# Kernel optimization log

Hardware: AMD Instinct MI355X
Metric: run time of the kernel (lower is better)

Reference implementation:

```python
import jax, jax.numpy as jnp
import numpy as np

D = 256          # d_model
NPRE = 16; NMLP = 16; NPOST = 16
K = 4            # top_k
P = NPRE * NMLP * NPOST   # 4096 pathways
HMAX = 5 * D     # max mlp expert hidden width (padded storage)
B, S = 8, 256


def _gelu(z):
    return jax.nn.gelu(z, approximate=False)  # torch nn.GELU default = exact erf


def _ln(z, g, b, eps=1e-5):
    mu = z.mean(-1, keepdims=True)
    v = ((z - mu) ** 2).mean(-1, keepdims=True)
    return (z - mu) * jax.lax.rsqrt(v + eps) * g + b


def setup_inputs() -> dict:
    key = jax.random.key(0)
    ks = jax.random.split(key, 8)

    def nrm(k, shape, scale):
        return jax.random.normal(k, shape, dtype=jnp.float32) * scale

    return {
        "x": nrm(ks[0], (B, S, D), 1.0),
        # router MLP (dropout inactive in eval)
        "rw1": nrm(ks[1], (D, 256), D ** -0.5), "rb1": jnp.zeros((256,), jnp.float32),
        "rw2": nrm(ks[2], (256, 128), 256 ** -0.5), "rb2": jnp.zeros((128,), jnp.float32),
        "rw3": nrm(ks[3], (128, P), 128 ** -0.5), "rb3": jnp.zeros((P,), jnp.float32),
        "temp": jnp.ones((1,), jnp.float32),
        # pre experts: Linear + LayerNorm + act
        "pw": nrm(ks[4], (NPRE, D, D), D ** -0.5), "pb": jnp.zeros((NPRE, D), jnp.float32),
        "pg": jnp.ones((NPRE, D), jnp.float32), "pbb": jnp.zeros((NPRE, D), jnp.float32),
        # mlp experts: variable hidden D*(2+i//4), padded to HMAX (unused cols sliced off)
        "mw1": nrm(ks[5], (NMLP, D, HMAX), D ** -0.5), "mb1": jnp.zeros((NMLP, HMAX), jnp.float32),
        "mw2": nrm(ks[6], (NMLP, HMAX, D), HMAX ** -0.5), "mb2": jnp.zeros((NMLP, D), jnp.float32),
        # post experts: Linear + (LayerNorm if even)
        "qw": nrm(ks[7], (NPOST, D, D), D ** -0.5), "qb": jnp.zeros((NPOST, D), jnp.float32),
        "qg": jnp.ones((NPOST, D), jnp.float32), "qbb": jnp.zeros((NPOST, D), jnp.float32),
    }


def reference(x, rw1, rb1, rw2, rb2, rw3, rb3, temp, pw, pb, pg, pbb,
              mw1, mb1, mw2, mb2, qw, qb, qg, qbb):
    Bv, Sv, Dv = x.shape
    N = Bv * Sv
    xt = x.reshape(N, Dv)

    # ---- router ----
    h = _gelu(xt @ rw1 + rb1)
    h = _gelu(h @ rw2 + rb2)
    scores = h @ rw3 + rb3                                  # [N, P]

    # ---- GLBL load-balance loss (softmax without temperature; torch.var unbiased) ----
    freq = jax.nn.softmax(scores, axis=-1).mean(0)          # [P]
    glbl_loss = P * jnp.var(freq, ddof=1)

    # ---- top-k pathway selection ----
    probs = jax.nn.softmax(scores / temp[0], axis=-1)
    top_vals, top_idx = jax.lax.top_k(probs, K)             # [N, K]
    pw_full = jnp.zeros((N, P), x.dtype).at[jnp.arange(N)[:, None], top_idx].set(top_vals)
    pathway_weights = pw_full / (pw_full.sum(-1, keepdims=True) + 1e-8)

    # ---- decompose pathway index -> (pre, mlp, post) ----
    pre_idx = top_idx // (NMLP * NPOST)
    rem = top_idx % (NMLP * NPOST)
    mlp_idx = rem // NPOST
    post_idx = rem % NPOST

    # ---- pre experts: compute all, gather per (token, slot) ----
    acts = [_gelu, jax.nn.relu, jnp.tanh]
    pre_all = jnp.stack(
        [acts[i % 3](_ln(xt @ pw[i] + pb[i], pg[i], pbb[i])) for i in range(NPRE)],
        axis=1)                                              # [N, NPRE, D]
    x_pre = jnp.take_along_axis(pre_all, pre_idx[:, :, None], axis=1)  # [N, K, D]

    # ---- mlp experts (variable hidden width), masked combine ----
    x_mlp = jnp.zeros_like(x_pre)
    for j in range(NMLP):
        hid = Dv * (2 + j // 4)
        a = _gelu if j % 2 == 0 else jax.nn.relu
        mid = a(jnp.einsum('nkd,dh->nkh', x_pre, mw1[j, :, :hid]) + mb1[j, :hid])
        out = jnp.einsum('nkh,hd->nkd', mid, mw2[j, :hid, :]) + mb2[j]
        x_mlp = x_mlp + jnp.where((mlp_idx == j)[:, :, None], out, 0.0)

    # ---- post experts, masked combine ----
    x_post = jnp.zeros_like(x_mlp)
    for q in range(NPOST):
        out = jnp.einsum('nkd,de->nke', x_mlp, qw[q]) + qb[q]
        if q % 2 == 0:
            out = _ln(out, qg[q], qbb[q])
        x_post = x_post + jnp.where((post_idx == q)[:, :, None], out, 0.0)

    # original weights each pathway by its (unnormalized) top value
    output = (x_post * top_vals[:, :, None]).sum(1).reshape(Bv, Sv, Dv)
    return output, glbl_loss, pathway_weights.reshape(Bv, Sv, P)
```

## Files before the change

### kernel.cpp

```cpp
#include <hip/hip_runtime.h>
#include <math.h>

#define DMODEL 256
#define PWAYS  4096
#define TOPK   4
#define HMAX   1280
#define NTOK   2048
#define NPAIR  (NTOK*TOPK)
#define FSLOTS 16
#define MROWS  64
#define YMLP   8
#define CTOT   56

typedef __attribute__((ext_vector_type(8))) short bf16x8;
typedef __attribute__((ext_vector_type(8))) unsigned short u16x8;
typedef __attribute__((ext_vector_type(4))) float f32x4;

#define MFMA_BF16 __builtin_amdgcn_mfma_f32_16x16x32_bf16

__device__ __forceinline__ float gelu_exact(float z) {
    return 0.5f * z * (1.0f + erff(z * 0.70710678118654752440f));
}

__device__ __forceinline__ unsigned short f32_to_bf16_rne(float f) {
    unsigned u = __float_as_uint(f);
    unsigned r = u + 0x7FFFu + ((u >> 16) & 1u);
    return (unsigned short)(r >> 16);
}

__device__ __forceinline__ float bf16_to_f32(unsigned short h) {
    return __uint_as_float((unsigned)h << 16);
}

__device__ __forceinline__ int chunk_base(int e) {
    int g = e >> 2, r = e & 3;
    return 4 * (2 * g + (g * (g - 1)) / 2) + r * (2 + g);
}


__global__ void k_zero(float* __restrict__ pwout, float* __restrict__ freq_part) {
    const int i = blockIdx.x * 256 + threadIdx.x;
    const int stride = gridDim.x * 256;
    for (int j = i; j < NTOK * PWAYS; j += stride) pwout[j] = 0.0f;
    for (int j = i; j < FSLOTS * PWAYS; j += stride) freq_part[j] = 0.0f;
}

__global__ void k_zero2(float* __restrict__ out, float* __restrict__ x_mlp,
                        int* __restrict__ cnts) {
    const int i = blockIdx.x * 256 + threadIdx.x;
    const int stride = gridDim.x * 256;
    for (int j = i; j < NTOK * DMODEL; j += stride) out[j] = 0.0f;
    for (int j = i; j < NPAIR * DMODEL; j += stride) x_mlp[j] = 0.0f;
    if (i < 192) cnts[i] = 0;
}

__global__ void __launch_bounds__(256) k_router_h(
    const float* __restrict__ x,
    const float* __restrict__ rw1, const float* __restrict__ rb1,
    const float* __restrict__ rw2, const float* __restrict__ rb2,
    unsigned short* __restrict__ h2h, unsigned short* __restrict__ h2l,
    unsigned short* __restrict__ xth, unsigned short* __restrict__ xtl) {
    __shared__ float xs[4][DMODEL];
    __shared__ float h1s[4][DMODEL];
    __shared__ float h2s[4][128];
    const int tid = threadIdx.x;
    const int n0 = blockIdx.x * 4;

    for (int idx = tid; idx < 4 * DMODEL; idx += 256) {
        const float v = x[(size_t)n0 * DMODEL + idx];
        xs[idx >> 8][idx & 255] = v;
        const unsigned short h = f32_to_bf16_rne(v);
        xth[(size_t)n0 * DMODEL + idx] = h;
        xtl[(size_t)n0 * DMODEL + idx] = f32_to_bf16_rne(v - bf16_to_f32(h));
    }
    __syncthreads();

    {
        float bias = rb1[tid];
        float a0 = bias, a1 = bias, a2 = bias, a3 = bias;
        for (int c = 0; c < DMODEL; c++) {
            float wv = rw1[c * DMODEL + tid];
            a0 += xs[0][c] * wv; a1 += xs[1][c] * wv;
            a2 += xs[2][c] * wv; a3 += xs[3][c] * wv;
        }
        h1s[0][tid] = gelu_exact(a0); h1s[1][tid] = gelu_exact(a1);
        h1s[2][tid] = gelu_exact(a2); h1s[3][tid] = gelu_exact(a3);
    }
    __syncthreads();

    {
        const int col = tid & 127;
        const int pr = tid >> 7;
        float bias = rb2[col];
        float b0 = bias, b1 = bias;
        for (int c = 0; c < DMODEL; c++) {
            float wv = rw2[c * 128 + col];
            b0 += h1s[2 * pr + 0][c] * wv;
            b1 += h1s[2 * pr + 1][c] * wv;
        }
        h2s[2 * pr + 0][col] = gelu_exact(b0);
        h2s[2 * pr + 1][col] = gelu_exact(b1);
    }
    __syncthreads();

    for (int idx = tid; idx < 512; idx += 256) {
        const int t = idx >> 7, col = idx & 127;
        const float v = h2s[t][col];
        const unsigned short h = f32_to_bf16_rne(v);
        const size_t o = (size_t)(n0 + t) * 128 + col;
        h2h[o] = h;
        h2l[o] = f32_to_bf16_rne(v - bf16_to_f32(h));
    }
}

__global__ void __launch_bounds__(256) k_pack3(
    const float* __restrict__ rw3, unsigned short* __restrict__ P3) {
    const int nb = blockIdx.x;
    const int tid = threadIdx.x;
    const int kb = tid >> 6, lane = tid & 63;
    const int l15 = lane & 15, lhi = lane >> 4;
    const int k0 = kb * 32 + lhi * 8;
    const int n = nb * 16 + l15;
    u16x8 hv, lv;
#pragma unroll
    for (int j = 0; j < 8; ++j) {
        const float f = rw3[(size_t)(k0 + j) * PWAYS + n];
        const unsigned short h = f32_to_bf16_rne(f);
        hv[j] = h;
        lv[j] = f32_to_bf16_rne(f - bf16_to_f32(h));
    }
    const size_t o0 = ((size_t)(0 * 256 + nb) * 4 + kb) * 512 + (size_t)lane * 8;
    const size_t o1 = ((size_t)(1 * 256 + nb) * 4 + kb) * 512 + (size_t)lane * 8;
    *(u16x8*)&P3[o0] = hv;
    *(u16x8*)&P3[o1] = lv;
}

__global__ void __launch_bounds__(256) k_packq(
    const float* __restrict__ pw, const float* __restrict__ qw,
    unsigned short* __restrict__ PPK, unsigned short* __restrict__ QPK) {
    const int e = blockIdx.x;
    const int which = blockIdx.y;
    const int kb = blockIdx.z;
    const int tid = threadIdx.x;
    const int wid = tid >> 6, lane = tid & 63;
    const int l15 = lane & 15, lhi = lane >> 4;
    const float* src = which ? qw : pw;
    unsigned short* dst = which ? QPK : PPK;

    for (int nb = wid; nb < 16; nb += 4) {
        const int n = nb * 16 + l15;
        const int k0 = kb * 32 + lhi * 8;
        u16x8 hv, lv;
#pragma unroll
        for (int j = 0; j < 8; ++j) {
            const float f = src[(size_t)e * DMODEL * DMODEL + (size_t)(k0 + j) * DMODEL + n];
            const unsigned short h = f32_to_bf16_rne(f);
            hv[j] = h;
            lv[j] = f32_to_bf16_rne(f - bf16_to_f32(h));
        }
        const size_t o0 = ((((size_t)e * 2 + 0) * 16 + nb) * 8 + kb) * 512 + (size_t)lane * 8;
        const size_t o1 = ((((size_t)e * 2 + 1) * 16 + nb) * 8 + kb) * 512 + (size_t)lane * 8;
        *(u16x8*)&dst[o0] = hv;
        *(u16x8*)&dst[o1] = lv;
    }
}

__global__ void __launch_bounds__(256, 2) k_scores(
    const unsigned short* __restrict__ h2h, const unsigned short* __restrict__ h2l,
    const unsigned short* __restrict__ P3, const float* __restrict__ rb3,
    float* __restrict__ scores) {
    const int n0 = blockIdx.x * 32;
    const int by = blockIdx.y;
    const int tid = threadIdx.x;
    const int wid = tid >> 6, lane = tid & 63;
    const int l15 = lane & 15, lhi = lane >> 4;

    __shared__ unsigned short ah[32][136];
    __shared__ unsigned short al[32][136];

    for (int t = tid; t < 512; t += 256) {
        const int row = t >> 4, seg = (t & 15) * 8;
        const size_t g = (size_t)(n0 + row) * 128 + seg;
        *(u16x8*)&ah[row][seg] = *(const u16x8*)&h2h[g];
        *(u16x8*)&al[row][seg] = *(const u16x8*)&h2l[g];
    }
    __syncthreads();

    f32x4 acc[2][4];
    const f32x4 zf = {0.f, 0.f, 0.f, 0.f};
#pragma unroll
    for (int ms = 0; ms < 2; ++ms)
#pragma unroll
        for (int ns = 0; ns < 4; ++ns) acc[ms][ns] = zf;

#pragma unroll 1
    for (int kb = 0; kb < 4; ++kb) {
        const int ko = kb * 32 + lhi * 8;
        const bf16x8 a_h0 = *(const bf16x8*)&ah[l15][ko];
        const bf16x8 a_h1 = *(const bf16x8*)&ah[16 + l15][ko];
        const bf16x8 a_l0 = *(const bf16x8*)&al[l15][ko];
        const bf16x8 a_l1 = *(const bf16x8*)&al[16 + l15][ko];
#pragma unroll
        for (int ns = 0; ns < 4; ++ns) {
            const int nb = by * 16 + wid * 4 + ns;
            const size_t bo = ((size_t)nb * 4 + kb) * 512 + (size_t)lane * 8;
            const bf16x8 bh = *(const bf16x8*)&P3[bo];
            const bf16x8 bl = *(const bf16x8*)&P3[bo + 524288];
            acc[0][ns] = MFMA_BF16(a_h0, bh, acc[0][ns], 0, 0, 0);
            acc[1][ns] = MFMA_BF16(a_h1, bh, acc[1][ns], 0, 0, 0);
            acc[0][ns] = MFMA_BF16(a_l0, bh, acc[0][ns], 0, 0, 0);
            acc[1][ns] = MFMA_BF16(a_l1, bh, acc[1][ns], 0, 0, 0);
            acc[0][ns] = MFMA_BF16(a_h0, bl, acc[0][ns], 0, 0, 0);
            acc[1][ns] = MFMA_BF16(a_h1, bl, acc[1][ns], 0, 0, 0);
        }
    }

#pragma unroll
    for (int ms = 0; ms < 2; ++ms)
#pragma unroll
        for (int ns = 0; ns < 4; ++ns) {
            const int col = by * 256 + wid * 64 + ns * 16 + l15;
            const float bias = rb3[col];
#pragma unroll
            for (int r = 0; r < 4; ++r) {
                const int row = n0 + ms * 16 + lhi * 4 + r;
                scores[(size_t)row * PWAYS + col] = acc[ms][ns][r] + bias;
            }
        }
}

__global__ void __launch_bounds__(256) k_topk(
    const float* __restrict__ scores, const float* __restrict__ temp,
    int* __restrict__ top_idx, float* __restrict__ top_vals,
    float* __restrict__ pw_out, float* __restrict__ tok_m, float* __restrict__ tok_i) {
    const int n = blockIdx.x;
    const int tid = threadIdx.x;
    const int wid = tid >> 6, lane = tid & 63;
    const float* row = scores + (size_t)n * PWAYS;

    float sv[16];
#pragma unroll
    for (int i = 0; i < 16; ++i) sv[i] = row[tid + i * 256];

    __shared__ float wred[4];
    __shared__ float wr1[4], wrT[4];
    __shared__ float wbv[4];
    __shared__ int wbi[4];
    __shared__ int sel[TOPK];
    __shared__ float selv[TOPK];

    float lmax = -3.402823466e38f;
#pragma unroll
    for (int i = 0; i < 16; ++i) lmax = fmaxf(lmax, sv[i]);
    for (int o = 32; o > 0; o >>= 1) lmax = fmaxf(lmax, __shfl_down(lmax, o));
    if (lane == 0) wred[wid] = lmax;
    __syncthreads();
    const float m = fmaxf(fmaxf(wred[0], wred[1]), fmaxf(wred[2], wred[3]));

    const float invT = 1.0f / temp[0];
    float e1 = 0.f, eT = 0.f;
#pragma unroll
    for (int i = 0; i < 16; ++i) {
        const float d = sv[i] - m;
        e1 += expf(d);
        eT += expf(d * invT);
    }
    for (int o = 32; o > 0; o >>= 1) { e1 += __shfl_down(e1, o); eT += __shfl_down(eT, o); }
    if (lane == 0) { wr1[wid] = e1; wrT[wid] = eT; }
    __syncthreads();
    const float sum1 = wr1[0] + wr1[1] + wr1[2] + wr1[3];
    const float sumT = wrT[0] + wrT[1] + wrT[2] + wrT[3];

    for (int r = 0; r < TOPK; ++r) {
        float bv = -3.402823466e38f;
        int bi = PWAYS;
#pragma unroll
        for (int i = 0; i < 16; ++i) {
            const int p = tid + i * 256;
            bool skip = false;
            for (int u = 0; u < r; ++u) if (sel[u] == p) skip = true;
            if (!skip && sv[i] > bv) { bv = sv[i]; bi = p; }
        }
        for (int o = 32; o > 0; o >>= 1) {
            const float ov = __shfl_down(bv, o);
            const int oi = __shfl_down(bi, o);
            if (ov > bv || (ov == bv && oi < bi)) { bv = ov; bi = oi; }
        }
        if (lane == 0) { wbv[wid] = bv; wbi[wid] = bi; }
        __syncthreads();
        if (tid == 0) {
            float b = wbv[0]; int bidx = wbi[0];
            for (int w = 1; w < 4; ++w)
                if (wbv[w] > b || (wbv[w] == b && wbi[w] < bidx)) { b = wbv[w]; bidx = wbi[w]; }
            sel[r] = bidx; selv[r] = b;
        }
        __syncthreads();
    }

    if (tid == 0) {
        float tv[TOPK];
        float wsum = 1e-8f;
#pragma unroll
        for (int k2 = 0; k2 < TOPK; ++k2) {
            tv[k2] = expf((selv[k2] - m) * invT) / sumT;
            wsum += tv[k2];
        }
        const float invw = 1.0f / wsum;
#pragma unroll
        for (int k2 = 0; k2 < TOPK; ++k2) {
            top_idx[n * TOPK + k2] = sel[k2];
            top_vals[n * TOPK + k2] = tv[k2];
            pw_out[(size_t)n * PWAYS + sel[k2]] = tv[k2] * invw;
        }
        tok_m[n] = m;
        tok_i[n] = 1.0f / sum1;
    }
}

__global__ void __launch_bounds__(256) k_freq(
    const float* __restrict__ scores, const float* __restrict__ tok_m,
    const float* __restrict__ tok_i, float* __restrict__ freq_part) {
    const int bx = blockIdx.x;
    const int by = blockIdx.y;
    const int tid = threadIdx.x;
    const int wid = tid >> 6, lane = tid & 63;
    const int col = bx * 64 + lane;

    float acc = 0.f;
    const int r0 = by * 128;
    for (int r = r0 + wid; r < r0 + 128; r += 4) {
        const float mm = tok_m[r], iv = tok_i[r];
        acc += expf(scores[(size_t)r * PWAYS + col] - mm) * iv;
    }
    __shared__ float fs[4][64];
    fs[wid][lane] = acc;
    __syncthreads();
    if (wid == 0)
        freq_part[(size_t)by * PWAYS + col] = fs[0][lane] + fs[1][lane] + fs[2][lane] + fs[3][lane];
}

__global__ void k_freq_loss(const float* __restrict__ freq_part, float* __restrict__ out_loss) {
    __shared__ float fl[PWAYS];
    __shared__ float red[256];
    const int tid = threadIdx.x;
    for (int p = tid; p < PWAYS; p += 256) {
        float s = 0.f;
        for (int sl = 0; sl < FSLOTS; sl++) s += freq_part[(size_t)sl * PWAYS + p];
        fl[p] = s * (1.0f / NTOK);
    }
    __syncthreads();
    float s = 0.f;
    for (int p = tid; p < PWAYS; p += 256) s += fl[p];
    red[tid] = s; __syncthreads();
    for (int st = 128; st > 0; st >>= 1) { if (tid < st) red[tid] += red[tid + st]; __syncthreads(); }
    const float mu = red[0] * (1.0f / PWAYS);
    __syncthreads();
    float ss = 0.f;
    for (int p = tid; p < PWAYS; p += 256) {
        float d = fl[p] - mu;
        ss += d * d;
    }
    red[tid] = ss; __syncthreads();
    for (int st = 128; st > 0; st >>= 1) { if (tid < st) red[tid] += red[tid + st]; __syncthreads(); }
    if (tid == 0)
        out_loss[0] = (float)PWAYS * red[0] / (float)(PWAYS - 1);
}


__global__ void k_count(const int* __restrict__ top_idx, int* __restrict__ counts) {
    const int p = blockIdx.x * 256 + threadIdx.x;
    if (p >= NPAIR) return;
    const int idx = top_idx[p];
    atomicAdd(&counts[0 * 16 + (idx >> 8)], 1);
    atomicAdd(&counts[1 * 16 + ((idx >> 4) & 15)], 1);
    atomicAdd(&counts[2 * 16 + (idx & 15)], 1);
}

__global__ void k_prefix(const int* __restrict__ counts, int* __restrict__ offsets,
                         int* __restrict__ cursors) {
    if (threadIdx.x != 0 || blockIdx.x != 0) return;
    for (int s = 0; s < 3; s++) {
        int run = 0;
        for (int e = 0; e < 16; e++) {
            offsets[s * 16 + e] = run;
            cursors[s * 16 + e] = run;
            run += counts[s * 16 + e];
        }
    }
}

__global__ void k_scatter(const int* __restrict__ top_idx, int* __restrict__ cursors,
                          int* __restrict__ lists) {
    const int p = blockIdx.x * 256 + threadIdx.x;
    if (p >= NPAIR) return;
    const int idx = top_idx[p];
    int pos;
    pos = atomicAdd(&cursors[0 * 16 + (idx >> 8)], 1);        lists[0 * NPAIR + pos] = p;
    pos = atomicAdd(&cursors[1 * 16 + ((idx >> 4) & 15)], 1); lists[1 * NPAIR + pos] = p;
    pos = atomicAdd(&cursors[2 * 16 + (idx & 15)], 1);        lists[2 * NPAIR + pos] = p;
}

__global__ void __launch_bounds__(256) k_packw(
    const float* __restrict__ mw1, const float* __restrict__ mw2,
    unsigned short* __restrict__ W1P, unsigned short* __restrict__ W2P) {
    const int cl = blockIdx.x;
    const int which = blockIdx.y;
    const int kb = blockIdx.z;
    int e = 0;
    while (e < 15 && chunk_base(e + 1) <= cl) ++e;
    const int ch = cl - chunk_base(e);
    const int hbase = ch * 256;
    const int tid = threadIdx.x;
    const int wid = tid >> 6, lane = tid & 63;
    const int l15 = lane & 15, lhi = lane >> 4;

    unsigned short* dst = which ? W2P : W1P;

    for (int nb = wid; nb < 16; nb += 4) {
        const int n = nb * 16 + l15;
        const int k0 = kb * 32 + lhi * 8;
        u16x8 hv, lv;
#pragma unroll
        for (int j = 0; j < 8; ++j) {
            float f;
            if (which == 0)
                f = mw1[((size_t)e * DMODEL + (k0 + j)) * HMAX + hbase + n];
            else
                f = mw2[((size_t)e * HMAX + hbase + k0 + j) * DMODEL + n];
            const unsigned short h = f32_to_bf16_rne(f);
            hv[j] = h;
            lv[j] = f32_to_bf16_rne(f - bf16_to_f32(h));
        }
        const size_t o0 = ((((size_t)cl * 2 + 0) * 16 + nb) * 8 + kb) * 512 + (size_t)lane * 8;
        const size_t o1 = ((((size_t)cl * 2 + 1) * 16 + nb) * 8 + kb) * 512 + (size_t)lane * 8;
        *(u16x8*)&dst[o0] = hv;
        *(u16x8*)&dst[o1] = lv;
    }
}

__global__ void __launch_bounds__(256) k_cvt(
    const float* __restrict__ src, unsigned short* __restrict__ dh,
    unsigned short* __restrict__ dl) {
    const size_t i = ((size_t)blockIdx.x * 256 + threadIdx.x) * 4;
    const float4 v = *(const float4*)&src[i];
    ushort4 hv, lv;
    hv.x = f32_to_bf16_rne(v.x); lv.x = f32_to_bf16_rne(v.x - bf16_to_f32(hv.x));
    hv.y = f32_to_bf16_rne(v.y); lv.y = f32_to_bf16_rne(v.y - bf16_to_f32(hv.y));
    hv.z = f32_to_bf16_rne(v.z); lv.z = f32_to_bf16_rne(v.z - bf16_to_f32(hv.z));
    hv.w = f32_to_bf16_rne(v.w); lv.w = f32_to_bf16_rne(v.w - bf16_to_f32(hv.w));
    *(ushort4*)&dh[i] = hv;
    *(ushort4*)&dl[i] = lv;
}

__global__ void __launch_bounds__(256, 2) k_pre_mfma(
    const unsigned short* __restrict__ xth, const unsigned short* __restrict__ xtl,
    const unsigned short* __restrict__ PPK,
    const float* __restrict__ pb, const float* __restrict__ pg, const float* __restrict__ pbb,
    const int* __restrict__ counts, const int* __restrict__ offsets,
    const int* __restrict__ lists,
    unsigned short* __restrict__ x_h, unsigned short* __restrict__ x_l) {
    const int e = blockIdx.x;
    const int cnt = counts[e];
    if (cnt == 0) return;
    const int off = offsets[e];
    const int am = e % 3;
    const int tid = threadIdx.x;
    const int wid = tid >> 6, lane = tid & 63;
    const int l15 = lane & 15, lhi = lane >> 4;

    __shared__ int prs[32];
    __shared__ unsigned short ah[32][264];
    __shared__ unsigned short al[32][264];
    __shared__ float s1s[4][32], s2s[4][32];
    __shared__ float mus[32], ivs[32];

    float bias4[4], g4[4], bb4[4];
#pragma unroll
    for (int ns = 0; ns < 4; ++ns) {
        const int col = wid * 64 + ns * 16 + l15;
        bias4[ns] = pb[e * DMODEL + col];
        g4[ns] = pg[e * DMODEL + col];
        bb4[ns] = pbb[e * DMODEL + col];
    }
    const size_t wbase = (size_t)e * 2 * 65536;

    for (int base = blockIdx.y * 32; base < cnt; base += 16 * 32) {
        const int Tact = min(32, cnt - base);
        if (tid < 32) prs[tid] = lists[off + base + min(tid, Tact - 1)];
        __syncthreads();
        for (int t = tid; t < 1024; t += 256) {
            const int row = t >> 5, seg = (t & 31) * 8;
            const size_t gsrc = (size_t)(prs[row] >> 2) * DMODEL + seg;
            *(uint4*)&ah[row][seg] = *(const uint4*)&xth[gsrc];
            *(uint4*)&al[row][seg] = *(const uint4*)&xtl[gsrc];
        }
        __syncthreads();

        f32x4 acc[2][4];
        const f32x4 zf = {0.f, 0.f, 0.f, 0.f};
#pragma unroll
        for (int ms = 0; ms < 2; ++ms)
#pragma unroll
            for (int ns = 0; ns < 4; ++ns) acc[ms][ns] = zf;

#pragma unroll 1
        for (int kb = 0; kb < 8; ++kb) {
            const int ko = kb * 32 + lhi * 8;
            const bf16x8 a_h0 = *(const bf16x8*)&ah[l15][ko];
            const bf16x8 a_h1 = *(const bf16x8*)&ah[16 + l15][ko];
            const bf16x8 a_l0 = *(const bf16x8*)&al[l15][ko];
            const bf16x8 a_l1 = *(const bf16x8*)&al[16 + l15][ko];
#pragma unroll
            for (int ns = 0; ns < 4; ++ns) {
                const size_t bo = wbase + (size_t)(((wid * 4 + ns) * 8 + kb) * 512 + lane * 8);
                const bf16x8 bh = *(const bf16x8*)&PPK[bo];
                const bf16x8 bl = *(const bf16x8*)&PPK[bo + 65536];
                acc[0][ns] = MFMA_BF16(a_h0, bh, acc[0][ns], 0, 0, 0);
                acc[1][ns] = MFMA_BF16(a_h1, bh, acc[1][ns], 0, 0, 0);
                acc[0][ns] = MFMA_BF16(a_l0, bh, acc[0][ns], 0, 0, 0);
                acc[1][ns] = MFMA_BF16(a_l1, bh, acc[1][ns], 0, 0, 0);
                acc[0][ns] = MFMA_BF16(a_h0, bl, acc[0][ns], 0, 0, 0);
                acc[1][ns] = MFMA_BF16(a_h1, bl, acc[1][ns], 0, 0, 0);
            }
        }

#pragma unroll
        for (int ms = 0; ms < 2; ++ms)
#pragma unroll
            for (int r = 0; r < 4; ++r) {
                float s1 = 0.f, s2 = 0.f;
#pragma unroll
                for (int ns = 0; ns < 4; ++ns) {
                    const float v = acc[ms][ns][r] + bias4[ns];
                    s1 += v; s2 += v * v;
                }
#pragma unroll
                for (int o = 1; o < 16; o <<= 1) {
                    s1 += __shfl_xor(s1, o);
                    s2 += __shfl_xor(s2, o);
                }
                if (l15 == 0) {
                    s1s[wid][ms * 16 + lhi * 4 + r] = s1;
                    s2s[wid][ms * 16 + lhi * 4 + r] = s2;
                }
            }
        __syncthreads();
        if (tid < 32) {
            const float s1 = s1s[0][tid] + s1s[1][tid] + s1s[2][tid] + s1s[3][tid];
            const float s2 = s2s[0][tid] + s2s[1][tid] + s2s[2][tid] + s2s[3][tid];
            const float mu = s1 * (1.0f / DMODEL);
            mus[tid] = mu;
            ivs[tid] = rsqrtf(s2 * (1.0f / DMODEL) - mu * mu + 1e-5f);
        }
        __syncthreads();

#pragma unroll
        for (int ms = 0; ms < 2; ++ms)
#pragma unroll
            for (int ns = 0; ns < 4; ++ns) {
                const int col = wid * 64 + ns * 16 + l15;
#pragma unroll
                for (int r = 0; r < 4; ++r) {
                    const int row = ms * 16 + lhi * 4 + r;
                    if (row < Tact) {
                        const float v = acc[ms][ns][r] + bias4[ns];
                        float y = (v - mus[row]) * ivs[row] * g4[ns] + bb4[ns];
                        y = (am == 0) ? gelu_exact(y) : (am == 1 ? fmaxf(y, 0.f) : tanhf(y));
                        const unsigned short h = f32_to_bf16_rne(y);
                        const size_t o = (size_t)prs[row] * DMODEL + col;
                        x_h[o] = h;
                        x_l[o] = f32_to_bf16_rne(y - bf16_to_f32(h));
                    }
                }
            }
        __syncthreads();
    }
}

__global__ void __launch_bounds__(256, 2) k_mlp_mfma(
    const unsigned short* __restrict__ x_h, const unsigned short* __restrict__ x_l,
    const unsigned short* __restrict__ W1P, const unsigned short* __restrict__ W2P,
    const float* __restrict__ mb1, const float* __restrict__ mb2,
    const int* __restrict__ counts, const int* __restrict__ offsets,
    const int* __restrict__ lists, float* __restrict__ x_mlp) {
    const int p = blockIdx.x & 7;
    const int j = blockIdx.x >> 3;
    const int ea = p;
    const int eb = (p < 4) ? (p + 12) : (p + 4);
    const int na = (2 + (ea >> 2)) * YMLP;
    int e, ch, y;
    if (j < na) { e = ea; ch = j >> 3; y = j & 7; }
    else        { e = eb; ch = (j - na) >> 3; y = (j - na) & 7; }

    const int cnt = counts[16 + e];
    if (cnt == 0) return;
    const int off = offsets[16 + e];
    const int cl = chunk_base(e) + ch;
    const bool is_gelu = ((e & 1) == 0);
    const int tid = threadIdx.x;
    const int wid = tid >> 6, lane = tid & 63;
    const int l15 = lane & 15, lhi = lane >> 4;

    __shared__ int prs[MROWS];
    __shared__ unsigned short ah[MROWS][264];
    __shared__ unsigned short al[MROWS][264];

    float hb_s[4], ob_s[4];
#pragma unroll
    for (int ns = 0; ns < 4; ++ns) {
        const int col = wid * 64 + ns * 16 + l15;
        hb_s[ns] = mb1[e * HMAX + ch * DMODEL + col];
        ob_s[ns] = (ch == 0) ? mb2[e * DMODEL + col] : 0.0f;
    }

    const size_t wbase = (size_t)cl * 2 * 65536;

    for (int base = y * MROWS; base < cnt; base += YMLP * MROWS) {
        const int Tact = min(MROWS, cnt - base);
        if (tid < MROWS) prs[tid] = lists[NPAIR + off + base + min(tid, Tact - 1)];
        __syncthreads();
        for (int t = tid; t < 2048; t += 256) {
            const int row = t >> 5, seg = (t & 31) * 8;
            const size_t gsrc = (size_t)prs[row] * DMODEL + seg;
            *(uint4*)&ah[row][seg] = *(const uint4*)&x_h[gsrc];
            *(uint4*)&al[row][seg] = *(const uint4*)&x_l[gsrc];
        }
        __syncthreads();

        {
            f32x4 acc[4][4];
            const f32x4 zf = {0.f, 0.f, 0.f, 0.f};
#pragma unroll
            for (int ms = 0; ms < 4; ++ms)
#pragma unroll
                for (int ns = 0; ns < 4; ++ns) acc[ms][ns] = zf;

#pragma unroll 1
            for (int kb = 0; kb < 8; ++kb) {
                const int ko = kb * 32 + lhi * 8;
#pragma unroll
                for (int ns = 0; ns < 4; ++ns) {
                    const size_t bo = wbase + (size_t)(((wid * 4 + ns) * 8 + kb) * 512 + lane * 8);
                    const bf16x8 bh = *(const bf16x8*)&W1P[bo];
                    const bf16x8 bl = *(const bf16x8*)&W1P[bo + 65536];
#pragma unroll
                    for (int ms = 0; ms < 4; ++ms) {
                        const bf16x8 a_h = *(const bf16x8*)&ah[ms * 16 + l15][ko];
                        const bf16x8 a_l = *(const bf16x8*)&al[ms * 16 + l15][ko];
                        acc[ms][ns] = MFMA_BF16(a_h, bh, acc[ms][ns], 0, 0, 0);
                        acc[ms][ns] = MFMA_BF16(a_l, bh, acc[ms][ns], 0, 0, 0);
                        acc[ms][ns] = MFMA_BF16(a_h, bl, acc[ms][ns], 0, 0, 0);
                    }
                }
            }
            __syncthreads();

#pragma unroll
            for (int ms = 0; ms < 4; ++ms)
#pragma unroll
                for (int ns = 0; ns < 4; ++ns) {
                    const int col = wid * 64 + ns * 16 + l15;
#pragma unroll
                    for (int r = 0; r < 4; ++r) {
                        const int row = ms * 16 + lhi * 4 + r;
                        float v = acc[ms][ns][r] + hb_s[ns];
                        v = is_gelu ? gelu_exact(v) : fmaxf(v, 0.0f);
                        const unsigned short h = f32_to_bf16_rne(v);
                        ah[row][col] = h;
                        al[row][col] = f32_to_bf16_rne(v - bf16_to_f32(h));
                    }
                }
            __syncthreads();
        }

        {
            f32x4 acc2[4][4];
            const f32x4 zf = {0.f, 0.f, 0.f, 0.f};
#pragma unroll
            for (int ms = 0; ms < 4; ++ms)
#pragma unroll
                for (int ns = 0; ns < 4; ++ns) acc2[ms][ns] = zf;

#pragma unroll 1
            for (int kb = 0; kb < 8; ++kb) {
                const int ko = kb * 32 + lhi * 8;
#pragma unroll
                for (int ns = 0; ns < 4; ++ns) {
                    const size_t bo = wbase + (size_t)(((wid * 4 + ns) * 8 + kb) * 512 + lane * 8);
                    const bf16x8 bh = *(const bf16x8*)&W2P[bo];
                    const bf16x8 bl = *(const bf16x8*)&W2P[bo + 65536];
#pragma unroll
                    for (int ms = 0; ms < 4; ++ms) {
                        const bf16x8 a_h = *(const bf16x8*)&ah[ms * 16 + l15][ko];
                        const bf16x8 a_l = *(const bf16x8*)&al[ms * 16 + l15][ko];
                        acc2[ms][ns] = MFMA_BF16(a_h, bh, acc2[ms][ns], 0, 0, 0);
                        acc2[ms][ns] = MFMA_BF16(a_l, bh, acc2[ms][ns], 0, 0, 0);
                        acc2[ms][ns] = MFMA_BF16(a_h, bl, acc2[ms][ns], 0, 0, 0);
                    }
                }
            }

#pragma unroll
            for (int ms = 0; ms < 4; ++ms)
#pragma unroll
                for (int ns = 0; ns < 4; ++ns) {
                    const int col = wid * 64 + ns * 16 + l15;
#pragma unroll
                    for (int r = 0; r < 4; ++r) {
                        const int row = ms * 16 + lhi * 4 + r;
                        if (row < Tact)
                            atomicAdd(&x_mlp[(size_t)prs[row] * DMODEL + col],
                                      acc2[ms][ns][r] + ob_s[ns]);
                    }
                }
        }
        __syncthreads();
    }
}

__global__ void __launch_bounds__(256, 2) k_post_mfma(
    const unsigned short* __restrict__ xmh, const unsigned short* __restrict__ xml,
    const unsigned short* __restrict__ QPK,
    const float* __restrict__ qb, const float* __restrict__ qg, const float* __restrict__ qbb,
    const float* __restrict__ top_val,
    const int* __restrict__ counts, const int* __restrict__ offsets,
    const int* __restrict__ lists, float* __restrict__ out) {
    const int e = blockIdx.x;
    const int cnt = counts[32 + e];
    if (cnt == 0) return;
    const int off = offsets[32 + e];
    const bool has_ln = ((e & 1) == 0);
    const int tid = threadIdx.x;
    const int wid = tid >> 6, lane = tid & 63;
    const int l15 = lane & 15, lhi = lane >> 4;

    __shared__ int prs[32];
    __shared__ float tvs[32];
    __shared__ unsigned short ah[32][264];
    __shared__ unsigned short al[32][264];
    __shared__ float s1s[4][32], s2s[4][32];
    __shared__ float mus[32], ivs[32];

    float bias4[4], g4[4], bb4[4];
#pragma unroll
    for (int ns = 0; ns < 4; ++ns) {
        const int col = wid * 64 + ns * 16 + l15;
        bias4[ns] = qb[e * DMODEL + col];
        g4[ns] = qg[e * DMODEL + col];
        bb4[ns] = qbb[e * DMODEL + col];
    }
    const size_t wbase = (size_t)e * 2 * 65536;

    for (int base = blockIdx.y * 32; base < cnt; base += 16 * 32) {
        const int Tact = min(32, cnt - base);
        if (tid < 32) {
            const int p = lists[2 * NPAIR + off + base + min(tid, Tact - 1)];
            prs[tid] = p;
            tvs[tid] = top_val[p];
        }
        __syncthreads();
        for (int t = tid; t < 1024; t += 256) {
            const int row = t >> 5, seg = (t & 31) * 8;
            const size_t gsrc = (size_t)prs[row] * DMODEL + seg;
            *(uint4*)&ah[row][seg] = *(const uint4*)&xmh[gsrc];
            *(uint4*)&al[row][seg] = *(const uint4*)&xml[gsrc];
        }
        __syncthreads();

        f32x4 acc[2][4];
        const f32x4 zf = {0.f, 0.f, 0.f, 0.f};
#pragma unroll
        for (int ms = 0; ms < 2; ++ms)
#pragma unroll
            for (int ns = 0; ns < 4; ++ns) acc[ms][ns] = zf;

#pragma unroll 1
        for (int kb = 0; kb < 8; ++kb) {
            const int ko = kb * 32 + lhi * 8;
            const bf16x8 a_h0 = *(const bf16x8*)&ah[l15][ko];
            const bf16x8 a_h1 = *(const bf16x8*)&ah[16 + l15][ko];
            const bf16x8 a_l0 = *(const bf16x8*)&al[l15][ko];
            const bf16x8 a_l1 = *(const bf16x8*)&al[16 + l15][ko];
#pragma unroll
            for (int ns = 0; ns < 4; ++ns) {
                const size_t bo = wbase + (size_t)(((wid * 4 + ns) * 8 + kb) * 512 + lane * 8);
                const bf16x8 bh = *(const bf16x8*)&QPK[bo];
                const bf16x8 bl = *(const bf16x8*)&QPK[bo + 65536];
                acc[0][ns] = MFMA_BF16(a_h0, bh, acc[0][ns], 0, 0, 0);
                acc[1][ns] = MFMA_BF16(a_h1, bh, acc[1][ns], 0, 0, 0);
                acc[0][ns] = MFMA_BF16(a_l0, bh, acc[0][ns], 0, 0, 0);
                acc[1][ns] = MFMA_BF16(a_l1, bh, acc[1][ns], 0, 0, 0);
                acc[0][ns] = MFMA_BF16(a_h0, bl, acc[0][ns], 0, 0, 0);
                acc[1][ns] = MFMA_BF16(a_h1, bl, acc[1][ns], 0, 0, 0);
            }
        }

        if (has_ln) {
#pragma unroll
            for (int ms = 0; ms < 2; ++ms)
#pragma unroll
                for (int r = 0; r < 4; ++r) {
                    float s1 = 0.f, s2 = 0.f;
#pragma unroll
                    for (int ns = 0; ns < 4; ++ns) {
                        const float v = acc[ms][ns][r] + bias4[ns];
                        s1 += v; s2 += v * v;
                    }
#pragma unroll
                    for (int o = 1; o < 16; o <<= 1) {
                        s1 += __shfl_xor(s1, o);
                        s2 += __shfl_xor(s2, o);
                    }
                    if (l15 == 0) {
                        s1s[wid][ms * 16 + lhi * 4 + r] = s1;
                        s2s[wid][ms * 16 + lhi * 4 + r] = s2;
                    }
                }
            __syncthreads();
            if (tid < 32) {
                const float s1 = s1s[0][tid] + s1s[1][tid] + s1s[2][tid] + s1s[3][tid];
                const float s2 = s2s[0][tid] + s2s[1][tid] + s2s[2][tid] + s2s[3][tid];
                const float mu = s1 * (1.0f / DMODEL);
                mus[tid] = mu;
                ivs[tid] = rsqrtf(s2 * (1.0f / DMODEL) - mu * mu + 1e-5f);
            }
            __syncthreads();
        }

#pragma unroll
        for (int ms = 0; ms < 2; ++ms)
#pragma unroll
            for (int ns = 0; ns < 4; ++ns) {
                const int col = wid * 64 + ns * 16 + l15;
#pragma unroll
                for (int r = 0; r < 4; ++r) {
                    const int row = ms * 16 + lhi * 4 + r;
                    if (row < Tact) {
                        const float v = acc[ms][ns][r] + bias4[ns];
                        const float t = has_ln ? ((v - mus[row]) * ivs[row] * g4[ns] + bb4[ns]) : v;
                        atomicAdd(&out[(size_t)(prs[row] >> 2) * DMODEL + col], tvs[row] * t);
                    }
                }
            }
        __syncthreads();
    }
}

extern "C" void kernel_launch(void* const* d_in, const int* in_sizes, int n_in,
                              void* d_out, int out_size, void* d_ws, size_t ws_size,
                              hipStream_t stream) {
    (void)in_sizes; (void)n_in; (void)out_size; (void)ws_size;

    const float* x    = (const float*)d_in[0];
    const float* rw1  = (const float*)d_in[1];
    const float* rb1  = (const float*)d_in[2];
    const float* rw2  = (const float*)d_in[3];
    const float* rb2  = (const float*)d_in[4];
    const float* rw3  = (const float*)d_in[5];
    const float* rb3  = (const float*)d_in[6];
    const float* temp = (const float*)d_in[7];
    const float* pw   = (const float*)d_in[8];
    const float* pb   = (const float*)d_in[9];
    const float* pg   = (const float*)d_in[10];
    const float* pbb  = (const float*)d_in[11];
    const float* mw1  = (const float*)d_in[12];
    const float* mb1  = (const float*)d_in[13];
    const float* mw2  = (const float*)d_in[14];
    const float* mb2  = (const float*)d_in[15];
    const float* qw   = (const float*)d_in[16];
    const float* qb   = (const float*)d_in[17];
    const float* qg   = (const float*)d_in[18];
    const float* qbb  = (const float*)d_in[19];

    float* out      = (float*)d_out;
    float* out_loss = out + (size_t)NTOK * DMODEL;
    float* out_pw   = out_loss + 1;

    float* freq_part = (float*)d_ws;
    int*   top_idx   = (int*)(freq_part + (size_t)FSLOTS * PWAYS);
    float* top_val   = (float*)(top_idx + NPAIR);
    int*   counts    = (int*)(top_val + NPAIR);
    int*   offsets   = counts + 64;
    int*   cursors   = offsets + 64;
    int*   lists     = cursors + 64;
    float* x_mlp     = (float*)(lists + 3 * NPAIR);
    unsigned short* x_h = (unsigned short*)(x_mlp + (size_t)NPAIR * DMODEL);
    unsigned short* x_l = x_h + (size_t)NPAIR * DMODEL;
    unsigned short* W1P = x_l + (size_t)NPAIR * DMODEL;
    unsigned short* W2P = W1P + (size_t)CTOT * 2 * 65536;
    unsigned short* P3  = W2P + (size_t)CTOT * 2 * 65536;
    unsigned short* h2h = P3 + 2 * 524288;
    unsigned short* h2l = h2h + (size_t)NTOK * 128;
    float* tok_m = (float*)(h2l + (size_t)NTOK * 128);
    float* tok_i = tok_m + NTOK;
    unsigned short* xth = (unsigned short*)(tok_i + NTOK);
    unsigned short* xtl = xth + (size_t)NTOK * DMODEL;
    unsigned short* xmh = xtl + (size_t)NTOK * DMODEL;
    unsigned short* xml = xmh + (size_t)NPAIR * DMODEL;
    unsigned short* PPK = xml + (size_t)NPAIR * DMODEL;
    unsigned short* QPK = PPK + (size_t)16 * 2 * 65536;
    float* scores = x_mlp;

    k_zero<<<1024, 256, 0, stream>>>(out_pw, freq_part);
    k_router_h<<<NTOK / 4, 256, 0, stream>>>(x, rw1, rb1, rw2, rb2, h2h, h2l, xth, xtl);
    k_pack3<<<256, 256, 0, stream>>>(rw3, P3);
    k_packq<<<dim3(16, 2, 8), 256, 0, stream>>>(pw, qw, PPK, QPK);
    k_scores<<<dim3(64, 16), 256, 0, stream>>>(h2h, h2l, P3, rb3, scores);
    k_topk<<<NTOK, 256, 0, stream>>>(scores, temp, top_idx, top_val, out_pw, tok_m, tok_i);
    k_freq<<<dim3(64, 16), 256, 0, stream>>>(scores, tok_m, tok_i, freq_part);
    k_freq_loss<<<1, 256, 0, stream>>>(freq_part, out_loss);

    k_zero2<<<1024, 256, 0, stream>>>(out, x_mlp, counts);
    k_count<<<NPAIR / 256, 256, 0, stream>>>(top_idx, counts);
    k_prefix<<<1, 64, 0, stream>>>(counts, offsets, cursors);
    k_scatter<<<NPAIR / 256, 256, 0, stream>>>(top_idx, cursors, lists);
    k_packw<<<dim3(CTOT, 2, 8), 256, 0, stream>>>(mw1, mw2, W1P, W2P);
    k_pre_mfma<<<dim3(16, 16), 256, 0, stream>>>(xth, xtl, PPK, pb, pg, pbb,
                                                 counts, offsets, lists, x_h, x_l);
    k_mlp_mfma<<<CTOT * YMLP, 256, 0, stream>>>(x_h, x_l, W1P, W2P, mb1, mb2,
                                                counts, offsets, lists, x_mlp);
    k_cvt<<<NPAIR * DMODEL / 1024, 256, 0, stream>>>(x_mlp, xmh, xml);
    k_post_mfma<<<dim3(16, 16), 256, 0, stream>>>(xmh, xml, QPK, qb, qg, qbb, top_val,
                                                  counts, offsets, lists, out);
}
```

Measured before the change: 518.8 us.

## Move router MLP to split-bf16 MFMA and fuse zeroing and conversion passes

The scalar fp32 router hidden layers are replaced with a split-bf16 (hi/lo) MFMA kernel, backed by new packing kernels for rw1/rw2 and a separate x conversion kernel. The zero-fill kernel for the pathway-weight output is dropped; the top-k kernel now writes each full output row, zeros included. The standalone x_mlp bf16 conversion pass is folded into the post-expert kernel's operand staging. The aim is to remove memory passes and slow scalar FMAs, at the cost of extra packing launches and the small error of the split-bf16 approximation.

```diff
diff --git a/kernel.cpp b/kernel.cpp
--- a/kernel.cpp
+++ b/kernel.cpp
@@ -38,13 +38,6 @@
 }
 
 
-__global__ void k_zero(float* __restrict__ pwout, float* __restrict__ freq_part) {
-    const int i = blockIdx.x * 256 + threadIdx.x;
-    const int stride = gridDim.x * 256;
-    for (int j = i; j < NTOK * PWAYS; j += stride) pwout[j] = 0.0f;
-    for (int j = i; j < FSLOTS * PWAYS; j += stride) freq_part[j] = 0.0f;
-}
-
 __global__ void k_zero2(float* __restrict__ out, float* __restrict__ x_mlp,
                         int* __restrict__ cnts) {
     const int i = blockIdx.x * 256 + threadIdx.x;
@@ -54,62 +47,168 @@
     if (i < 192) cnts[i] = 0;
 }
 
-__global__ void __launch_bounds__(256) k_router_h(
-    const float* __restrict__ x,
-    const float* __restrict__ rw1, const float* __restrict__ rb1,
-    const float* __restrict__ rw2, const float* __restrict__ rb2,
-    unsigned short* __restrict__ h2h, unsigned short* __restrict__ h2l,
-    unsigned short* __restrict__ xth, unsigned short* __restrict__ xtl) {
-    __shared__ float xs[4][DMODEL];
-    __shared__ float h1s[4][DMODEL];
-    __shared__ float h2s[4][128];
-    const int tid = threadIdx.x;
-    const int n0 = blockIdx.x * 4;
-
-    for (int idx = tid; idx < 4 * DMODEL; idx += 256) {
-        const float v = x[(size_t)n0 * DMODEL + idx];
-        xs[idx >> 8][idx & 255] = v;
-        const unsigned short h = f32_to_bf16_rne(v);
-        xth[(size_t)n0 * DMODEL + idx] = h;
-        xtl[(size_t)n0 * DMODEL + idx] = f32_to_bf16_rne(v - bf16_to_f32(h));
+__global__ void __launch_bounds__(256) k_cvtx(
+    const float* __restrict__ src, unsigned short* __restrict__ dh,
+    unsigned short* __restrict__ dl) {
+    const size_t i = ((size_t)blockIdx.x * 256 + threadIdx.x) * 4;
+    const float4 v = *(const float4*)&src[i];
+    ushort4 hv, lv;
+    hv.x = f32_to_bf16_rne(v.x); lv.x = f32_to_bf16_rne(v.x - bf16_to_f32(hv.x));
+    hv.y = f32_to_bf16_rne(v.y); lv.y = f32_to_bf16_rne(v.y - bf16_to_f32(hv.y));
+    hv.z = f32_to_bf16_rne(v.z); lv.z = f32_to_bf16_rne(v.z - bf16_to_f32(hv.z));
+    hv.w = f32_to_bf16_rne(v.w); lv.w = f32_to_bf16_rne(v.w - bf16_to_f32(hv.w));
+    *(ushort4*)&dh[i] = hv;
+    *(ushort4*)&dl[i] = lv;
+}
+
+__global__ void __launch_bounds__(256) k_pack12(
+    const float* __restrict__ rw1, const float* __restrict__ rw2,
+    unsigned short* __restrict__ R1P, unsigned short* __restrict__ R2P) {
+    const int bx = blockIdx.x;
+    const int tid = threadIdx.x;
+    const int kq = tid >> 6, lane = tid & 63;
+    const int l15 = lane & 15, lhi = lane >> 4;
+    const bool is1 = (bx < 16);
+    const int nb = is1 ? bx : (bx - 16);
+    const int N = is1 ? 256 : 128;
+    const float* src = is1 ? rw1 : rw2;
+    unsigned short* dst = is1 ? R1P : R2P;
+    const int nblk = is1 ? 16 : 8;
+    const int pstride = nblk * 8 * 512;
+    const int n = nb * 16 + l15;
+
+    for (int k2 = 0; k2 < 2; ++k2) {
+        const int kb = kq + k2 * 4;
+        const int k0 = kb * 32 + lhi * 8;
+        u16x8 hv, lv;
+#pragma unroll
+        for (int j = 0; j < 8; ++j) {
+            const float f = src[(size_t)(k0 + j) * N + n];
+            const unsigned short h = f32_to_bf16_rne(f);
+            hv[j] = h;
+            lv[j] = f32_to_bf16_rne(f - bf16_to_f32(h));
+        }
+        const size_t o = ((size_t)nb * 8 + kb) * 512 + (size_t)lane * 8;
+        *(u16x8*)&dst[o] = hv;
+        *(u16x8*)&dst[o + pstride] = lv;
+    }
+}
+
+__global__ void __launch_bounds__(256, 2) k_h12(
+    const unsigned short* __restrict__ xth, const unsigned short* __restrict__ xtl,
+    const unsigned short* __restrict__ R1P, const unsigned short* __restrict__ R2P,
+    const float* __restrict__ rb1, const float* __restrict__ rb2,
+    unsigned short* __restrict__ h2h, unsigned short* __restrict__ h2l) {
+    const int n0 = blockIdx.x * 32;
+    const int tid = threadIdx.x;
+    const int wid = tid >> 6, lane = tid & 63;
+    const int l15 = lane & 15, lhi = lane >> 4;
+
+    __shared__ unsigned short ah[32][264];
+    __shared__ unsigned short al[32][264];
+
+    for (int t = tid; t < 1024; t += 256) {
+        const int row = t >> 5, seg = (t & 31) * 8;
+        const size_t g = (size_t)(n0 + row) * DMODEL + seg;
+        *(u16x8*)&ah[row][seg] = *(const u16x8*)&xth[g];
+        *(u16x8*)&al[row][seg] = *(const u16x8*)&xtl[g];
     }
     __syncthreads();
 
     {
-        float bias = rb1[tid];
-        float a0 = bias, a1 = bias, a2 = bias, a3 = bias;
-        for (int c = 0; c < DMODEL; c++) {
-            float wv = rw1[c * DMODEL + tid];
-            a0 += xs[0][c] * wv; a1 += xs[1][c] * wv;
-            a2 += xs[2][c] * wv; a3 += xs[3][c] * wv;
-        }
-        h1s[0][tid] = gelu_exact(a0); h1s[1][tid] = gelu_exact(a1);
-        h1s[2][tid] = gelu_exact(a2); h1s[3][tid] = gelu_exact(a3);
-    }
-    __syncthreads();
+        f32x4 acc[2][4];
+        const f32x4 zf = {0.f, 0.f, 0.f, 0.f};
+#pragma unroll
+        for (int ms = 0; ms < 2; ++ms)
+#pragma unroll
+            for (int ns = 0; ns < 4; ++ns) acc[ms][ns] = zf;
+
+#pragma unroll 1
+        for (int kb = 0; kb < 8; ++kb) {
+            const int ko = kb * 32 + lhi * 8;
+            const bf16x8 a_h0 = *(const bf16x8*)&ah[l15][ko];
+            const bf16x8 a_h1 = *(const bf16x8*)&ah[16 + l15][ko];
+            const bf16x8 a_l0 = *(const bf16x8*)&al[l15][ko];
+            const bf16x8 a_l1 = *(const bf16x8*)&al[16 + l15][ko];
+#pragma unroll
+            for (int ns = 0; ns < 4; ++ns) {
+                const size_t bo = ((size_t)(wid * 4 + ns) * 8 + kb) * 512 + (size_t)lane * 8;
+                const bf16x8 bh = *(const bf16x8*)&R1P[bo];
+                const bf16x8 bl = *(const bf16x8*)&R1P[bo + 65536];
+                acc[0][ns] = MFMA_BF16(a_h0, bh, acc[0][ns], 0, 0, 0);
+                acc[1][ns] = MFMA_BF16(a_h1, bh, acc[1][ns], 0, 0, 0);
+                acc[0][ns] = MFMA_BF16(a_l0, bh, acc[0][ns], 0, 0, 0);
+                acc[1][ns] = MFMA_BF16(a_l1, bh, acc[1][ns], 0, 0, 0);
+                acc[0][ns] = MFMA_BF16(a_h0, bl, acc[0][ns], 0, 0, 0);
+                acc[1][ns] = MFMA_BF16(a_h1, bl, acc[1][ns], 0, 0, 0);
+            }
+        }
+        __syncthreads();
+
+#pragma unroll
+        for (int ms = 0; ms < 2; ++ms)
+#pragma unroll
+            for (int ns = 0; ns < 4; ++ns) {
+                const int col = wid * 64 + ns * 16 + l15;
+                const float bias = rb1[col];
+#pragma unroll
+                for (int r = 0; r < 4; ++r) {
+                    const int row = ms * 16 + lhi * 4 + r;
+                    const float v = gelu_exact(acc[ms][ns][r] + bias);
+                    const unsigned short h = f32_to_bf16_rne(v);
+                    ah[row][col] = h;
+                    al[row][col] = f32_to_bf16_rne(v - bf16_to_f32(h));
+                }
+            }
+        __syncthreads();
+    }
 
     {
-        const int col = tid & 127;
-        const int pr = tid >> 7;
-        float bias = rb2[col];
-        float b0 = bias, b1 = bias;
-        for (int c = 0; c < DMODEL; c++) {
-            float wv = rw2[c * 128 + col];
-            b0 += h1s[2 * pr + 0][c] * wv;
-            b1 += h1s[2 * pr + 1][c] * wv;
-        }
-        h2s[2 * pr + 0][col] = gelu_exact(b0);
-        h2s[2 * pr + 1][col] = gelu_exact(b1);
-    }
-    __syncthreads();
-
-    for (int idx = tid; idx < 512; idx += 256) {
-        const int t = idx >> 7, col = idx & 127;
-        const float v = h2s[t][col];
-        const unsigned short h = f32_to_bf16_rne(v);
-        const size_t o = (size_t)(n0 + t) * 128 + col;
-        h2h[o] = h;
-        h2l[o] = f32_to_bf16_rne(v - bf16_to_f32(h));
+        f32x4 acc2[2][2];
+        const f32x4 zf = {0.f, 0.f, 0.f, 0.f};
+#pragma unroll
+        for (int ms = 0; ms < 2; ++ms)
+#pragma unroll
+            for (int ns = 0; ns < 2; ++ns) acc2[ms][ns] = zf;
+
+#pragma unroll 1
+        for (int kb = 0; kb < 8; ++kb) {
+            const int ko = kb * 32 + lhi * 8;
+            const bf16x8 a_h0 = *(const bf16x8*)&ah[l15][ko];
+            const bf16x8 a_h1 = *(const bf16x8*)&ah[16 + l15][ko];
+            const bf16x8 a_l0 = *(const bf16x8*)&al[l15][ko];
+            const bf16x8 a_l1 = *(const bf16x8*)&al[16 + l15][ko];
+#pragma unroll
+            for (int ns = 0; ns < 2; ++ns) {
+                const int nb = wid * 2 + ns;
+                const size_t bo = ((size_t)nb * 8 + kb) * 512 + (size_t)lane * 8;
+                const bf16x8 bh = *(const bf16x8*)&R2P[bo];
+                const bf16x8 bl = *(const bf16x8*)&R2P[bo + 32768];
+                acc2[0][ns] = MFMA_BF16(a_h0, bh, acc2[0][ns], 0, 0, 0);
+                acc2[1][ns] = MFMA_BF16(a_h1, bh, acc2[1][ns], 0, 0, 0);
+                acc2[0][ns] = MFMA_BF16(a_l0, bh, acc2[0][ns], 0, 0, 0);
+                acc2[1][ns] = MFMA_BF16(a_l1, bh, acc2[1][ns], 0, 0, 0);
+                acc2[0][ns] = MFMA_BF16(a_h0, bl, acc2[0][ns], 0, 0, 0);
+                acc2[1][ns] = MFMA_BF16(a_h1, bl, acc2[1][ns], 0, 0, 0);
+            }
+        }
+
+#pragma unroll
+        for (int ms = 0; ms < 2; ++ms)
+#pragma unroll
+            for (int ns = 0; ns < 2; ++ns) {
+                const int col = wid * 32 + ns * 16 + l15;
+                const float bias = rb2[col];
+#pragma unroll
+                for (int r = 0; r < 4; ++r) {
+                    const int row = ms * 16 + lhi * 4 + r;
+                    const float v = gelu_exact(acc2[ms][ns][r] + bias);
+                    const unsigned short h = f32_to_bf16_rne(v);
+                    const size_t o = (size_t)(n0 + row) * 128 + col;
+                    h2h[o] = h;
+                    h2l[o] = f32_to_bf16_rne(v - bf16_to_f32(h));
+                }
+            }
     }
 }
 
@@ -248,6 +347,7 @@
     __shared__ int wbi[4];
     __shared__ int sel[TOPK];
     __shared__ float selv[TOPK];
+    __shared__ float pwv[TOPK];
 
     float lmax = -3.402823466e38f;
 #pragma unroll
@@ -310,10 +410,20 @@
         for (int k2 = 0; k2 < TOPK; ++k2) {
             top_idx[n * TOPK + k2] = sel[k2];
             top_vals[n * TOPK + k2] = tv[k2];
-            pw_out[(size_t)n * PWAYS + sel[k2]] = tv[k2] * invw;
+            pwv[k2] = tv[k2] * invw;
         }
         tok_m[n] = m;
         tok_i[n] = 1.0f / sum1;
+    }
+    __syncthreads();
+
+#pragma unroll
+    for (int i = 0; i < 16; ++i) {
+        const int p = tid + i * 256;
+        float v = 0.0f;
+#pragma unroll
+        for (int r = 0; r < TOPK; ++r) if (p == sel[r]) v = pwv[r];
+        pw_out[(size_t)n * PWAYS + p] = v;
     }
 }
 
@@ -436,20 +546,6 @@
         *(u16x8*)&dst[o0] = hv;
         *(u16x8*)&dst[o1] = lv;
     }
-}
-
-__global__ void __launch_bounds__(256) k_cvt(
-    const float* __restrict__ src, unsigned short* __restrict__ dh,
-    unsigned short* __restrict__ dl) {
-    const size_t i = ((size_t)blockIdx.x * 256 + threadIdx.x) * 4;
-    const float4 v = *(const float4*)&src[i];
-    ushort4 hv, lv;
-    hv.x = f32_to_bf16_rne(v.x); lv.x = f32_to_bf16_rne(v.x - bf16_to_f32(hv.x));
-    hv.y = f32_to_bf16_rne(v.y); lv.y = f32_to_bf16_rne(v.y - bf16_to_f32(hv.y));
-    hv.z = f32_to_bf16_rne(v.z); lv.z = f32_to_bf16_rne(v.z - bf16_to_f32(hv.z));
-    hv.w = f32_to_bf16_rne(v.w); lv.w = f32_to_bf16_rne(v.w - bf16_to_f32(hv.w));
-    *(ushort4*)&dh[i] = hv;
-    *(ushort4*)&dl[i] = lv;
 }
 
 __global__ void __launch_bounds__(256, 2) k_pre_mfma(
@@ -719,7 +815,7 @@
 }
 
 __global__ void __launch_bounds__(256, 2) k_post_mfma(
-    const unsigned short* __restrict__ xmh, const unsigned short* __restrict__ xml,
+    const float* __restrict__ x_mlp,
     const unsigned short* __restrict__ QPK,
     const float* __restrict__ qb, const float* __restrict__ qg, const float* __restrict__ qbb,
     const float* __restrict__ top_val,
@@ -761,9 +857,19 @@
         __syncthreads();
         for (int t = tid; t < 1024; t += 256) {
             const int row = t >> 5, seg = (t & 31) * 8;
-            const size_t gsrc = (size_t)prs[row] * DMODEL + seg;
-            *(uint4*)&ah[row][seg] = *(const uint4*)&xmh[gsrc];
-            *(uint4*)&al[row][seg] = *(const uint4*)&xml[gsrc];
+            const float* src = &x_mlp[(size_t)prs[row] * DMODEL + seg];
+            const float4 v0 = *(const float4*)&src[0];
+            const float4 v1 = *(const float4*)&src[4];
+            u16x8 hv, lv;
+            const float fv[8] = {v0.x, v0.y, v0.z, v0.w, v1.x, v1.y, v1.z, v1.w};
+#pragma unroll
+            for (int jj = 0; jj < 8; ++jj) {
+                const unsigned short h = f32_to_bf16_rne(fv[jj]);
+                hv[jj] = h;
+                lv[jj] = f32_to_bf16_rne(fv[jj] - bf16_to_f32(h));
+            }
+            *(u16x8*)&ah[row][seg] = hv;
+            *(u16x8*)&al[row][seg] = lv;
         }
         __syncthreads();
 
@@ -895,16 +1001,17 @@
     float* tok_i = tok_m + NTOK;
     unsigned short* xth = (unsigned short*)(tok_i + NTOK);
     unsigned short* xtl = xth + (size_t)NTOK * DMODEL;
-    unsigned short* xmh = xtl + (size_t)NTOK * DMODEL;
-    unsigned short* xml = xmh + (size_t)NPAIR * DMODEL;
-    unsigned short* PPK = xml + (size_t)NPAIR * DMODEL;
+    unsigned short* PPK = xtl + (size_t)NTOK * DMODEL;
     unsigned short* QPK = PPK + (size_t)16 * 2 * 65536;
+    unsigned short* R1P = QPK + (size_t)16 * 2 * 65536;
+    unsigned short* R2P = R1P + 2 * 65536;
     float* scores = x_mlp;
 
-    k_zero<<<1024, 256, 0, stream>>>(out_pw, freq_part);
-    k_router_h<<<NTOK / 4, 256, 0, stream>>>(x, rw1, rb1, rw2, rb2, h2h, h2l, xth, xtl);
+    k_cvtx<<<NTOK * DMODEL / 1024, 256, 0, stream>>>(x, xth, xtl);
+    k_pack12<<<24, 256, 0, stream>>>(rw1, rw2, R1P, R2P);
     k_pack3<<<256, 256, 0, stream>>>(rw3, P3);
     k_packq<<<dim3(16, 2, 8), 256, 0, stream>>>(pw, qw, PPK, QPK);
+    k_h12<<<NTOK / 32, 256, 0, stream>>>(xth, xtl, R1P, R2P, rb1, rb2, h2h, h2l);
     k_scores<<<dim3(64, 16), 256, 0, stream>>>(h2h, h2l, P3, rb3, scores);
     k_topk<<<NTOK, 256, 0, stream>>>(scores, temp, top_idx, top_val, out_pw, tok_m, tok_i);
     k_freq<<<dim3(64, 16), 256, 0, stream>>>(scores, tok_m, tok_i, freq_part);
@@ -919,7 +1026,6 @@
                                                  counts, offsets, lists, x_h, x_l);
     k_mlp_mfma<<<CTOT * YMLP, 256, 0, stream>>>(x_h, x_l, W1P, W2P, mb1, mb2,
                                                 counts, offsets, lists, x_mlp);
-    k_cvt<<<NPAIR * DMODEL / 1024, 256, 0, stream>>>(x_mlp, xmh, xml);
-    k_post_mfma<<<dim3(16, 16), 256, 0, stream>>>(xmh, xml, QPK, qb, qg, qbb, top_val,
+    k_post_mfma<<<dim3(16, 16), 256, 0, stream>>>(x_mlp, QPK, qb, qg, qbb, top_val,
                                                   counts, offsets, lists, out);
 }
```

Result: faster. 501.1 us (-3.4%).
